# Performance work log

Hardware: AMD Instinct MI355X
Metric: run time of the kernel (lower is better)

The kernel has to match this reference:

```python
import jax, jax.numpy as jnp
import numpy as np
import math

EPS = 1e-08
KERNEL = 3
PAD = KERNEL // 2


def setup_inputs() -> dict:
    key = jax.random.key(0)
    k1, k2, k3, k4 = jax.random.split(key, 4)
    B, C_in, C_out, H, W, S = 8, 512, 512, 64, 64, 512
    x = jax.random.normal(k1, (B, C_in, H, W), dtype=jnp.float32)
    style = jax.random.normal(k2, (B, S), dtype=jnp.float32)
    # modulation Linear: kaiming_normal fan_in linear => std = 1/sqrt(S); bias filled with 1
    w_mod = jax.random.normal(k3, (C_in, S), dtype=jnp.float32) / math.sqrt(S)
    b_mod = jnp.ones((C_in,), dtype=jnp.float32)
    # conv weight: randn / sqrt(in * k^2)
    weight = jax.random.normal(k4, (1, C_out, C_in, KERNEL, KERNEL), dtype=jnp.float32) / math.sqrt(C_in * KERNEL * KERNEL)
    return {"x": x, "style": style, "w_mod": w_mod, "b_mod": b_mod, "weight": weight}


def _modconv(x, style, w_mod, b_mod, weight):
    # style modulation: (B, S) @ (S, C_in) + bias -> (B, 1, C_in, 1, 1)
    s = style @ w_mod.T + b_mod
    w = weight * s[:, None, :, None, None]            # (B, C_out, C_in, k, k)
    # demodulate: rsqrt of sum of squares over (in, kh, kw)
    demod = jax.lax.rsqrt(jnp.sum(w * w, axis=(2, 3, 4)) + EPS)  # (B, C_out)
    w = w * demod[:, :, None, None, None]

    # groups=B conv == per-sample conv; vmap over batch
    def conv1(xb, wb):
        # xb: (C_in, H, W), wb: (C_out, C_in, k, k)
        return jax.lax.conv_general_dilated(
            xb[None], wb, window_strides=(1, 1),
            padding=[(PAD, PAD), (PAD, PAD)],
            dimension_numbers=("NCHW", "OIHW", "NCHW"))[0]

    return jax.vmap(conv1)(x, w)  # (B, C_out, H, W)


def reference(x, style, w_mod, b_mod, weight):
    return _modconv(x, style, w_mod, b_mod, weight)
```

## Files before the change

### kernel.cpp

```cpp
#include <hip/hip_runtime.h>
#include <hip/hip_bf16.h>

#define BATCH 8
#define CIN   512
#define COUT  512
#define HH    64
#define WW    64
#define SS    512
#define HP    66
#define WP    66
#define NPIX  (HH*WW)

typedef __bf16 bfrag  __attribute__((ext_vector_type(8)));
typedef float  f32x4  __attribute__((ext_vector_type(4)));
typedef unsigned short u16x8 __attribute__((ext_vector_type(8)));

__device__ __forceinline__ void async_copy16(const __hip_bfloat16* g, __hip_bfloat16* l) {
    __builtin_amdgcn_global_load_lds(
        (const __attribute__((address_space(1))) void*)g,
        (__attribute__((address_space(3))) void*)l,
        16, 0, 0);
}

__device__ __forceinline__ bool is_f32(const void* b_mod) {
    return ((const unsigned int*)b_mod)[0] == 0x3F800000u;
}

__global__ void k_prep(const void* __restrict__ style,
                       const void* __restrict__ w_mod,
                       const void* __restrict__ b_mod,
                       const void* __restrict__ weight,
                       float* __restrict__ s_out,
                       float* __restrict__ wsq,
                       __hip_bfloat16* __restrict__ Wt) {
    const bool f32 = is_f32(b_mod);
    if (blockIdx.x < 1024) {
        int tid = blockIdx.x * 256 + threadIdx.x;
        float sq = 0.f;
        if (f32) {
            const float* w = (const float*)weight + (size_t)tid * 9;
#pragma unroll
            for (int k = 0; k < 9; ++k) {
                float v = w[k];
                sq += v * v;
                Wt[k * (COUT * CIN) + tid] = __float2bfloat16(v);
            }
        } else {
            const __hip_bfloat16* w = (const __hip_bfloat16*)weight + (size_t)tid * 9;
#pragma unroll
            for (int k = 0; k < 9; ++k) {
                float v = __bfloat162float(w[k]);
                sq += v * v;
                Wt[k * (COUT * CIN) + tid] = w[k];
            }
        }
        wsq[tid] = sq;
    } else {
        int gw   = (blockIdx.x - 1024) * 4 + (threadIdx.x >> 6);
        int lane = threadIdx.x & 63;
        int b = gw >> 9, i = gw & 511;
        int base = lane * 8;
        float acc = 0.f;
        if (f32) {
            const float* st = (const float*)style + b * SS + base;
            const float* wm = (const float*)w_mod + i * SS + base;
#pragma unroll
            for (int j = 0; j < 8; ++j) acc += st[j] * wm[j];
        } else {
            const __hip_bfloat16* st = (const __hip_bfloat16*)style + b * SS + base;
            const __hip_bfloat16* wm = (const __hip_bfloat16*)w_mod + i * SS + base;
#pragma unroll
            for (int j = 0; j < 8; ++j)
                acc += __bfloat162float(st[j]) * __bfloat162float(wm[j]);
        }
#pragma unroll
        for (int off = 32; off; off >>= 1) acc += __shfl_down(acc, off);
        if (lane == 0) {
            float bias = f32 ? ((const float*)b_mod)[i]
                             : __bfloat162float(((const __hip_bfloat16*)b_mod)[i]);
            s_out[gw] = acc + bias;
        }
    }
}

__global__ void k_mid(const void* __restrict__ xv,
                      const float* __restrict__ s_buf,
                      const float* __restrict__ wsq,
                      const void* __restrict__ b_mod,
                      float* __restrict__ demod,
                      int b0, int nx, int do_demod,
                      __hip_bfloat16* __restrict__ xpad) {
    if ((int)blockIdx.x >= nx) {
        if (!do_demod) return;
        int gw   = ((int)blockIdx.x - nx) * 4 + (threadIdx.x >> 6);
        int lane = threadIdx.x & 63;
        int b = gw >> 9, o = gw & 511;
        int base = lane * 8;
        const float* sp = s_buf + b * CIN + base;
        const float* wp = wsq + o * CIN + base;
        float acc = 0.f;
#pragma unroll
        for (int j = 0; j < 8; ++j) {
            float sv = sp[j];
            acc += sv * sv * wp[j];
        }
#pragma unroll
        for (int off = 32; off; off >>= 1) acc += __shfl_down(acc, off);
        if (lane == 0) demod[gw] = rsqrtf(acc + 1e-8f);
        return;
    }
    const bool f32 = is_f32(b_mod);
    int ic = blockIdx.x & 15;
    int h  = (blockIdx.x >> 4) & 63;
    int bl = blockIdx.x >> 10;
    int b  = b0 + bl;
    int t  = threadIdx.x;
    int g  = t & 3;
    int w  = t >> 2;
    int ch0 = ic * 32 + g * 8;

    float sv[8];
#pragma unroll
    for (int j = 0; j < 8; ++j) sv[j] = s_buf[b * CIN + ch0 + j];

    u16x8 outv;
#pragma unroll
    for (int j = 0; j < 8; ++j) {
        size_t src = (size_t)(b * CIN + ch0 + j) * NPIX + h * WW + w;
        float xval = f32 ? ((const float*)xv)[src]
                         : __bfloat162float(((const __hip_bfloat16*)xv)[src]);
        __hip_bfloat16 bv = __float2bfloat16(xval * sv[j]);
        outv[j] = *(unsigned short*)&bv;
    }
    size_t rowb = (size_t)(bl * HP + h + 1) * WP;
    *(u16x8*)(xpad + (rowb + (w + 1)) * CIN + ch0) = outv;

    u16x8 z = {};
    if (w == 0)  *(u16x8*)(xpad + (rowb + 0)  * CIN + ch0) = z;
    if (w == 63) *(u16x8*)(xpad + (rowb + 65) * CIN + ch0) = z;
    if (h == 0) {
        size_t r0 = (size_t)(bl * HP + 0) * WP;
        *(u16x8*)(xpad + (r0 + (w + 1)) * CIN + ch0) = z;
        if (w == 0)  *(u16x8*)(xpad + (r0 + 0)  * CIN + ch0) = z;
        if (w == 63) *(u16x8*)(xpad + (r0 + 65) * CIN + ch0) = z;
    }
    if (h == 63) {
        size_t r65 = (size_t)(bl * HP + 65) * WP;
        *(u16x8*)(xpad + (r65 + (w + 1)) * CIN + ch0) = z;
        if (w == 0)  *(u16x8*)(xpad + (r65 + 0)  * CIN + ch0) = z;
        if (w == 63) *(u16x8*)(xpad + (r65 + 65) * CIN + ch0) = z;
    }
}

__global__ __launch_bounds__(256, 4)
void k_conv(const __hip_bfloat16* __restrict__ Wt,
            const __hip_bfloat16* __restrict__ xpad,
            const float* __restrict__ demod,
            const void* __restrict__ b_mod, int b0,
            void* __restrict__ outv) {
    __shared__ __hip_bfloat16 sA[3][128 * 32];
    __shared__ __hip_bfloat16 sB[6144];

    const int t    = threadIdx.x;
    const int wid  = t >> 6;
    const int lane = t & 63;
    const int p_tile = blockIdx.x;
    const int o_tile = blockIdx.y;
    const int bl     = blockIdx.z;
    const int b      = b0 + bl;

    const int o_base = o_tile * 128;
    const int h0     = p_tile * 2;
    const int p_base = p_tile * 128;

    const int acol = (lane & 3) * 8;
    const int arow0 = wid * 32 + (lane >> 2);
    const int arow1 = arow0 + 16;
    const int aoff0 = arow0 * 32 + acol;
    const int aoff1 = arow1 * 32 + acol;
    const int asrc0 = (o_base + arow0) * CIN + acol;
    const int asrc1 = (o_base + arow1) * CIN + acol;

    int bdst[3], bsrc[3];
#pragma unroll
    for (int jj = 0; jj < 3; ++jj) {
        int j   = wid * 3 + jj;
        int pix = j * 16 + (lane >> 2);
        int pm  = pix < 131 ? pix : 131;
        int r   = (pm >= 66) ? 1 : 0;
        int c   = pm - (r ? 66 : 0);
        bdst[jj] = j * 512 + lane * 8;
        bsrc[jj] = ((bl * HP + h0 + r) * WP + c) * CIN + (lane & 3) * 8;
    }

    const int quad   = lane >> 4;
    const int l15    = lane & 15;
    const int wave_m = (wid >> 1) * 64;
    const int wave_n = (wid & 1) * 64;
    int afrag[4], bfragoff[4];
#pragma unroll
    for (int mt = 0; mt < 4; ++mt)
        afrag[mt] = (wave_m + mt * 16 + l15) * 32 + quad * 8;
#pragma unroll
    for (int nt = 0; nt < 4; ++nt) {
        int n = wave_n + nt * 16 + l15;
        bfragoff[nt] = ((n >> 6) * 66 + (n & 63)) * 32 + quad * 8;
    }

    f32x4 acc[4][4];
#pragma unroll
    for (int mt = 0; mt < 4; ++mt)
#pragma unroll
        for (int nt = 0; nt < 4; ++nt)
            acc[mt][nt] = (f32x4)0.f;

    for (int kh = 0; kh < 3; ++kh) {
        const __hip_bfloat16* Wkh = Wt + kh * 3 * (COUT * CIN);
        const __hip_bfloat16* xr  = xpad + kh * (WP * CIN);
        for (int i0 = 0; i0 < CIN; i0 += 32) {
            __syncthreads();
#pragma unroll
            for (int kw = 0; kw < 3; ++kw) {
                const __hip_bfloat16* Ap = Wkh + kw * (COUT * CIN) + i0;
                async_copy16(Ap + asrc0, &sA[kw][aoff0]);
                async_copy16(Ap + asrc1, &sA[kw][aoff1]);
            }
#pragma unroll
            for (int jj = 0; jj < 3; ++jj)
                async_copy16(xr + bsrc[jj] + i0, sB + bdst[jj]);
            __syncthreads();

#pragma unroll
            for (int kw = 0; kw < 3; ++kw) {
                bfrag a[4], bb[4];
#pragma unroll
                for (int mt = 0; mt < 4; ++mt)
                    a[mt] = *(const bfrag*)(&sA[kw][afrag[mt]]);
#pragma unroll
                for (int nt = 0; nt < 4; ++nt)
                    bb[nt] = *(const bfrag*)(sB + bfragoff[nt] + kw * 32);
#pragma unroll
                for (int mt = 0; mt < 4; ++mt)
#pragma unroll
                    for (int nt = 0; nt < 4; ++nt)
                        acc[mt][nt] = __builtin_amdgcn_mfma_f32_16x16x32_bf16(
                            a[mt], bb[nt], acc[mt][nt], 0, 0, 0);
            }
        }
    }

    const bool f32 = is_f32(b_mod);
#pragma unroll
    for (int mt = 0; mt < 4; ++mt) {
        const int o0r = o_base + wave_m + mt * 16 + quad * 4;
        float dm[4];
#pragma unroll
        for (int r = 0; r < 4; ++r) dm[r] = demod[b * COUT + o0r + r];
#pragma unroll
        for (int nt = 0; nt < 4; ++nt) {
            const int p = p_base + wave_n + nt * 16 + l15;
#pragma unroll
            for (int r = 0; r < 4; ++r) {
                float val = acc[mt][nt][r] * dm[r];
                size_t idx = (size_t)(b * COUT + o0r + r) * NPIX + p;
                if (f32) ((float*)outv)[idx] = val;
                else     ((__hip_bfloat16*)outv)[idx] = __float2bfloat16(val);
            }
        }
    }
}

extern "C" void kernel_launch(void* const* d_in, const int* in_sizes, int n_in,
                              void* d_out, int out_size, void* d_ws, size_t ws_size,
                              hipStream_t stream) {
    const void* x      = d_in[0];
    const void* style  = d_in[1];
    const void* w_mod  = d_in[2];
    const void* b_mod  = d_in[3];
    const void* weight = d_in[4];

    char* ws = (char*)d_ws;
    float*          s_buf = (float*)(ws + 4096);
    float*          demod = (float*)(ws + 20480);
    float*          wsq   = (float*)(ws + 36864);
    __hip_bfloat16* Wt    = (__hip_bfloat16*)(ws + 1085440);
    __hip_bfloat16* xpad  = (__hip_bfloat16*)(ws + 5804032);

    const size_t need_full = 5804032 + (size_t)BATCH * HP * WP * CIN * 2;
    const int group = (ws_size >= need_full) ? 8 : 4;

    k_prep<<<2048, 256, 0, stream>>>(style, w_mod, b_mod, weight, s_buf, wsq, Wt);

    for (int b0 = 0; b0 < BATCH; b0 += group) {
        const int nx = 1024 * group;
        const int do_demod = (b0 == 0) ? 1 : 0;
        const int nd = do_demod ? 1024 : 0;
        k_mid<<<nx + nd, 256, 0, stream>>>(x, s_buf, wsq, b_mod, demod,
                                           b0, nx, do_demod, xpad);
        k_conv<<<dim3(32, 4, group), 256, 0, stream>>>(Wt, xpad, demod, b_mod, b0, d_out);
    }
}
```

Measured before the change: 274.4 us.

## Double-buffer conv LDS tiles with async prefetch and XOR-swizzled layout

Converts the single-buffered load-then-compute loop into a two-stage pipeline. The next K-slice is issued via global_load_lds into a second LDS buffer while MFMAs run on the current one, and a partial vmcnt wait replaces the full barrier drain. It also XOR-swizzles the 32-element LDS rows to reduce bank conflicts on fragment reads and raises wave priority during compute. LDS use doubles, so the occupancy hint drops from 4 to 2 blocks per CU, which trades latency hiding across blocks for overlap within a block.

```diff
diff --git a/kernel.cpp b/kernel.cpp
--- a/kernel.cpp
+++ b/kernel.cpp
@@ -152,18 +152,18 @@
     }
 }
 
-__global__ __launch_bounds__(256, 4)
+__global__ __launch_bounds__(256, 2)
 void k_conv(const __hip_bfloat16* __restrict__ Wt,
             const __hip_bfloat16* __restrict__ xpad,
             const float* __restrict__ demod,
             const void* __restrict__ b_mod, int b0,
             void* __restrict__ outv) {
-    __shared__ __hip_bfloat16 sA[3][128 * 32];
-    __shared__ __hip_bfloat16 sB[6144];
-
-    const int t    = threadIdx.x;
-    const int wid  = t >> 6;
-    const int lane = t & 63;
+    __shared__ __hip_bfloat16 sA[2][3][128 * 32];
+    __shared__ __hip_bfloat16 sB[2][6144];
+
+    const int tid  = threadIdx.x;
+    const int wid  = tid >> 6;
+    const int lane = tid & 63;
     const int p_tile = blockIdx.x;
     const int o_tile = blockIdx.y;
     const int bl     = blockIdx.z;
@@ -173,13 +173,14 @@
     const int h0     = p_tile * 2;
     const int p_base = p_tile * 128;
 
-    const int acol = (lane & 3) * 8;
+    const int sw = ((lane & 3) ^ ((lane >> 3) & 3)) * 8;
+
     const int arow0 = wid * 32 + (lane >> 2);
     const int arow1 = arow0 + 16;
-    const int aoff0 = arow0 * 32 + acol;
-    const int aoff1 = arow1 * 32 + acol;
-    const int asrc0 = (o_base + arow0) * CIN + acol;
-    const int asrc1 = (o_base + arow1) * CIN + acol;
+    const int aoff0 = wid * 1024 + lane * 8;
+    const int aoff1 = aoff0 + 512;
+    const int asrc0 = (o_base + arow0) * CIN + sw;
+    const int asrc1 = (o_base + arow1) * CIN + sw;
 
     int bdst[3], bsrc[3];
 #pragma unroll
@@ -190,21 +191,29 @@
         int r   = (pm >= 66) ? 1 : 0;
         int c   = pm - (r ? 66 : 0);
         bdst[jj] = j * 512 + lane * 8;
-        bsrc[jj] = ((bl * HP + h0 + r) * WP + c) * CIN + (lane & 3) * 8;
+        bsrc[jj] = ((bl * HP + h0 + r) * WP + c) * CIN + sw;
     }
 
     const int quad   = lane >> 4;
     const int l15    = lane & 15;
     const int wave_m = (wid >> 1) * 64;
     const int wave_n = (wid & 1) * 64;
-    int afrag[4], bfragoff[4];
-#pragma unroll
-    for (int mt = 0; mt < 4; ++mt)
-        afrag[mt] = (wave_m + mt * 16 + l15) * 32 + quad * 8;
+    int afrag[4];
+#pragma unroll
+    for (int mt = 0; mt < 4; ++mt) {
+        int row = wave_m + mt * 16 + l15;
+        afrag[mt] = row * 32 + ((quad ^ ((l15 >> 1) & 3)) * 8);
+    }
+    int bfroff[4][3];
 #pragma unroll
     for (int nt = 0; nt < 4; ++nt) {
-        int n = wave_n + nt * 16 + l15;
-        bfragoff[nt] = ((n >> 6) * 66 + (n & 63)) * 32 + quad * 8;
+        int n   = wave_n + nt * 16 + l15;
+        int pr0 = (n >> 6) * 66 + (n & 63);
+#pragma unroll
+        for (int kw = 0; kw < 3; ++kw) {
+            int pr = pr0 + kw;
+            bfroff[nt][kw] = pr * 32 + ((quad ^ ((pr >> 1) & 3)) * 8);
+        }
     }
 
     f32x4 acc[4][4];
@@ -214,40 +223,58 @@
         for (int nt = 0; nt < 4; ++nt)
             acc[mt][nt] = (f32x4)0.f;
 
-    for (int kh = 0; kh < 3; ++kh) {
-        const __hip_bfloat16* Wkh = Wt + kh * 3 * (COUT * CIN);
-        const __hip_bfloat16* xr  = xpad + kh * (WP * CIN);
-        for (int i0 = 0; i0 < CIN; i0 += 32) {
-            __syncthreads();
-#pragma unroll
-            for (int kw = 0; kw < 3; ++kw) {
-                const __hip_bfloat16* Ap = Wkh + kw * (COUT * CIN) + i0;
-                async_copy16(Ap + asrc0, &sA[kw][aoff0]);
-                async_copy16(Ap + asrc1, &sA[kw][aoff1]);
-            }
-#pragma unroll
-            for (int jj = 0; jj < 3; ++jj)
-                async_copy16(xr + bsrc[jj] + i0, sB + bdst[jj]);
-            __syncthreads();
-
-#pragma unroll
-            for (int kw = 0; kw < 3; ++kw) {
-                bfrag a[4], bb[4];
-#pragma unroll
-                for (int mt = 0; mt < 4; ++mt)
-                    a[mt] = *(const bfrag*)(&sA[kw][afrag[mt]]);
+    auto stage = [&](int buf, int it) {
+        const int kh = it >> 4;
+        const int i0 = (it & 15) << 5;
+        const __hip_bfloat16* Wkh = Wt + kh * 3 * (COUT * CIN) + i0;
+        const __hip_bfloat16* xr  = xpad + kh * (WP * CIN) + i0;
+#pragma unroll
+        for (int kw = 0; kw < 3; ++kw) {
+            const __hip_bfloat16* Ap = Wkh + kw * (COUT * CIN);
+            async_copy16(Ap + asrc0, &sA[buf][kw][aoff0]);
+            async_copy16(Ap + asrc1, &sA[buf][kw][aoff1]);
+        }
+#pragma unroll
+        for (int jj = 0; jj < 3; ++jj)
+            async_copy16(xr + bsrc[jj], &sB[buf][bdst[jj]]);
+    };
+
+    auto compute = [&](int buf) {
+        __builtin_amdgcn_s_setprio(1);
+#pragma unroll
+        for (int kw = 0; kw < 3; ++kw) {
+            bfrag a[4], bb[4];
+#pragma unroll
+            for (int mt = 0; mt < 4; ++mt)
+                a[mt] = *(const bfrag*)(&sA[buf][kw][afrag[mt]]);
+#pragma unroll
+            for (int nt = 0; nt < 4; ++nt)
+                bb[nt] = *(const bfrag*)(&sB[buf][bfroff[nt][kw]]);
+#pragma unroll
+            for (int mt = 0; mt < 4; ++mt)
 #pragma unroll
                 for (int nt = 0; nt < 4; ++nt)
-                    bb[nt] = *(const bfrag*)(sB + bfragoff[nt] + kw * 32);
-#pragma unroll
-                for (int mt = 0; mt < 4; ++mt)
-#pragma unroll
-                    for (int nt = 0; nt < 4; ++nt)
-                        acc[mt][nt] = __builtin_amdgcn_mfma_f32_16x16x32_bf16(
-                            a[mt], bb[nt], acc[mt][nt], 0, 0, 0);
-            }
-        }
-    }
+                    acc[mt][nt] = __builtin_amdgcn_mfma_f32_16x16x32_bf16(
+                        a[mt], bb[nt], acc[mt][nt], 0, 0, 0);
+        }
+        __builtin_amdgcn_s_setprio(0);
+    };
+
+    stage(0, 0);
+#pragma unroll 2
+    for (int it = 0; it < 47; ++it) {
+        stage((it + 1) & 1, it + 1);
+        asm volatile("s_waitcnt vmcnt(9)" ::: "memory");
+        __builtin_amdgcn_s_barrier();
+        asm volatile("" ::: "memory");
+        compute(it & 1);
+        asm volatile("" ::: "memory");
+        __builtin_amdgcn_s_barrier();
+    }
+    asm volatile("s_waitcnt vmcnt(0)" ::: "memory");
+    __builtin_amdgcn_s_barrier();
+    asm volatile("" ::: "memory");
+    compute(1);
 
     const bool f32 = is_f32(b_mod);
 #pragma unroll
```

Measured after the change: 269.0 us. About the same (-2.0%).
